# Kernel optimization log

Hardware: AMD Instinct MI355X
Metric: run time of the kernel (lower is better)

Reference implementation:

```python
import jax, jax.numpy as jnp
import numpy as np
from jax import lax

T_LOW, T_HIGH = 100.0, 200.0   # init kwargs of Canny
TG22 = 0.4142135623730951      # tan(22.5 deg), cv2's direction quantization constant
MAX_ITERS = 512                # safety cap on hysteresis fixed-point loop


def _shift(a, dy, dx):
    # neighbor value n[y, x] = a[y + dy, x + dx], zero outside
    H, W = a.shape
    p = jnp.pad(a, 1)
    return p[1 + dy:1 + dy + H, 1 + dx:1 + dx + W]


def _canny(x):
    B, C, H, W = x.shape
    # toRGB: ((x+1)/2*255).to(uint8)  (truncation; values are non-negative)
    img = jnp.clip(jnp.floor((x + 1.0) * 0.5 * 255.0), 0.0, 255.0)
    # original reshapes batch into one tall strip (B*H, W, C) before cv2.Canny
    img = img.transpose(0, 2, 3, 1).reshape(B * H, W, C)
    HH = B * H
    p = jnp.pad(img, ((1, 1), (1, 1), (0, 0)), mode='edge')  # replicate border like cv2

    def s(dy, dx):
        return p[1 + dy:1 + dy + HH, 1 + dx:1 + dx + W, :]

    # 3x3 Sobel per channel
    gx = (s(-1, 1) + 2.0 * s(0, 1) + s(1, 1)) - (s(-1, -1) + 2.0 * s(0, -1) + s(1, -1))
    gy = (s(1, -1) + 2.0 * s(1, 0) + s(1, 1)) - (s(-1, -1) + 2.0 * s(-1, 0) + s(-1, 1))
    mag_c = jnp.abs(gx) + jnp.abs(gy)  # L1 magnitude (cv2 default L2gradient=False)
    # multi-channel: take channel with max magnitude per pixel (cv2 behavior)
    idx = jnp.argmax(mag_c, axis=-1, keepdims=True)
    gx = jnp.take_along_axis(gx, idx, -1)[..., 0]
    gy = jnp.take_along_axis(gy, idx, -1)[..., 0]
    mag = jnp.take_along_axis(mag_c, idx, -1)[..., 0]

    # non-maximum suppression with 4 quantized directions
    ax_, ay_ = jnp.abs(gx), jnp.abs(gy)
    is_h = ay_ < TG22 * ax_          # gradient ~horizontal -> compare left/right
    is_v = ay_ * TG22 > ax_          # gradient ~vertical -> compare up/down
    same = (gx * gy) >= 0.0          # diagonal orientation by sign agreement
    n1 = jnp.where(is_h, _shift(mag, 0, -1),
         jnp.where(is_v, _shift(mag, -1, 0),
         jnp.where(same, _shift(mag, -1, -1), _shift(mag, -1, 1))))
    n2 = jnp.where(is_h, _shift(mag, 0, 1),
         jnp.where(is_v, _shift(mag, 1, 0),
         jnp.where(same, _shift(mag, 1, 1), _shift(mag, 1, -1))))
    keep = (mag > n1) & (mag >= n2)

    strong = keep & (mag > T_HIGH)
    weak = keep & (mag > T_LOW)

    # hysteresis: propagate strong labels through 8-connected weak pixels to fixed point
    def dilate(m):
        mf = m.astype(jnp.float32)
        return lax.reduce_window(mf, 0.0, lax.add, (3, 3), (1, 1), 'SAME') > 0.0

    def body(st):
        s0, _, it = st
        grown = (dilate(s0) & weak) | s0
        return grown, jnp.any(grown != s0), it + 1

    def cond(st):
        return st[1] & (st[2] < MAX_ITERS)

    strong, _, _ = lax.while_loop(cond, body, (strong, jnp.array(True), jnp.array(0)))

    edges = strong.reshape(B, H, W).astype(jnp.float32)        # {0,1} == cv2 {0,255}/255
    edges = jnp.broadcast_to(edges[:, None, :, :], (B, 3, H, W))
    return (edges - 0.5) / 0.5                                 # T.Normalize(0.5, 0.5)


def setup_inputs() -> dict:
    key = jax.random.key(0)
    x = jax.random.uniform(key, (16, 3, 512, 512), jnp.float32, -1.0, 1.0)
    return {"x": x}


def reference(x):
    return _canny(x)
```

## Files before the change

kernel.cpp:

```cpp
#include <hip/hip_runtime.h>
#include <stdint.h>

#define HH 8192
#define WW 512
#define WPR 8
#define TG22F 0.4142135623730951f
#define NROUND 8
#define NBLK 32


__device__ __forceinline__ float to_img(float v) {
    float t = floorf((v + 1.0f) * 0.5f * 255.0f);
    return fminf(fmaxf(t, 0.0f), 255.0f);
}

__device__ __forceinline__ uint64_t runfill(uint64_t s, uint64_t w) {
    uint64_t sw = s & w;
    uint64_t up = ((sw + w) ^ w) & w;
    uint64_t rs = __brevll(sw);
    uint64_t rw = __brevll(w);
    uint64_t dn = __brevll(((rs + rw) ^ rw) & rw);
    return up | dn | sw;
}

__device__ __forceinline__ uint64_t shfl_up64(uint64_t v, int d) {
    int lo = __shfl_up((int)(uint32_t)v, d, 64);
    int hi = __shfl_up((int)(uint32_t)(v >> 32), d, 64);
    return ((uint64_t)(uint32_t)hi << 32) | (uint32_t)lo;
}
__device__ __forceinline__ uint64_t shfl_dn64(uint64_t v, int d) {
    int lo = __shfl_down((int)(uint32_t)v, d, 64);
    int hi = __shfl_down((int)(uint32_t)(v >> 32), d, 64);
    return ((uint64_t)(uint32_t)hi << 32) | (uint32_t)lo;
}

__device__ __forceinline__ uint64_t cload64(const unsigned long long* p) {
    return __hip_atomic_load((const unsigned long long*)p, __ATOMIC_RELAXED,
                             __HIP_MEMORY_SCOPE_AGENT);
}
__device__ __forceinline__ void cstore64(unsigned long long* p, uint64_t v) {
    __hip_atomic_store(p, (unsigned long long)v, __ATOMIC_RELAXED,
                       __HIP_MEMORY_SCOPE_AGENT);
}

__device__ __forceinline__ void load_row10(const float* __restrict__ in,
                                           int row, int c, int lane, int a[10]) {
    const float* p = &in[(size_t)((((row >> 9) * 3 + c) << 9) + (row & 511)) << 9];
    const int x0 = lane << 3;
    float4 v0 = *(const float4*)&p[x0];
    float4 v1 = *(const float4*)&p[x0 + 4];
    a[1] = (int)(uint8_t)to_img(v0.x);
    a[2] = (int)(uint8_t)to_img(v0.y);
    a[3] = (int)(uint8_t)to_img(v0.z);
    a[4] = (int)(uint8_t)to_img(v0.w);
    a[5] = (int)(uint8_t)to_img(v1.x);
    a[6] = (int)(uint8_t)to_img(v1.y);
    a[7] = (int)(uint8_t)to_img(v1.z);
    a[8] = (int)(uint8_t)to_img(v1.w);
    int l = __shfl_up(a[8], 1, 64);
    a[0] = (lane == 0) ? a[1] : l;
    int r = __shfl_down(a[1], 1, 64);
    a[9] = (lane == 63) ? a[8] : r;
}

__global__ void k_sobel(const float* __restrict__ in, uint16_t* __restrict__ packed) {
    const int lane = threadIdx.x & 63;
    const int y  = (blockIdx.x << 2) + (threadIdx.x >> 6);
    const int ym = (y > 0) ? y - 1 : 0;
    const int yp = (y < HH - 1) ? y + 1 : HH - 1;

    int bestMag[8], bgx[8], bgy[8];
    #pragma unroll
    for (int j = 0; j < 8; ++j) { bestMag[j] = -1; bgx[j] = 0; bgy[j] = 0; }

    #pragma unroll
    for (int c = 0; c < 3; ++c) {
        int a0[10], a1[10], a2[10];
        load_row10(in, ym, c, lane, a0);
        load_row10(in, y,  c, lane, a1);
        load_row10(in, yp, c, lane, a2);
        int vs[10];
        #pragma unroll
        for (int i = 0; i < 10; ++i) vs[i] = a0[i] + 2 * a1[i] + a2[i];
        #pragma unroll
        for (int j = 0; j < 8; ++j) {
            int gx = vs[j + 2] - vs[j];
            int gy = (a2[j] + 2 * a2[j + 1] + a2[j + 2]) - (a0[j] + 2 * a0[j + 1] + a0[j + 2]);
            int mg = abs(gx) + abs(gy);
            if (mg > bestMag[j]) { bestMag[j] = mg; bgx[j] = gx; bgy[j] = gy; }
        }
    }

    uint32_t res[4];
    #pragma unroll
    for (int jj = 0; jj < 4; ++jj) {
        uint32_t pair = 0;
        #pragma unroll
        for (int s = 0; s < 2; ++s) {
            int j = jj * 2 + s;
            float axf = (float)abs(bgx[j]);
            float ayf = (float)abs(bgy[j]);
            int dir;
            if (ayf < TG22F * axf)      dir = 0;
            else if (ayf * TG22F > axf) dir = 1;
            else                        dir = (bgx[j] * bgy[j] >= 0) ? 2 : 3;
            uint32_t val = (uint32_t)(bestMag[j] | (dir << 12));
            pair |= val << (s * 16);
        }
        res[jj] = pair;
    }
    *(uint4*)&packed[y * WW + (lane << 3)] = *(uint4*)res;
}

#define MEXT(lo, hi, idx) ((int)((((idx) < 4 ? ((lo) >> (16 * (idx))) \
                                             : ((hi) >> (16 * ((idx) - 4))))) & 0xFFF))

__global__ void k_nms(const uint16_t* __restrict__ packed,
                      unsigned long long* __restrict__ strongB,
                      unsigned long long* __restrict__ weakB,
                      int* __restrict__ flags) {
    if (blockIdx.x == 0 && threadIdx.x < 16) flags[threadIdx.x] = 0;
    const int lane = threadIdx.x & 63;
    const int w = threadIdx.x >> 6;
    const int y = (blockIdx.x << 2) + w;

    uint4 q = *(const uint4*)&packed[y * WW + (lane << 3)];
    uint64_t oLo = ((uint64_t)q.y << 32) | q.x;
    uint64_t oHi = ((uint64_t)q.w << 32) | q.z;
    uint64_t uLo = 0, uHi = 0, dLo = 0, dHi = 0;
    if (y > 0) {
        uint4 qu = *(const uint4*)&packed[(y - 1) * WW + (lane << 3)];
        uLo = ((uint64_t)qu.y << 32) | qu.x;
        uHi = ((uint64_t)qu.w << 32) | qu.z;
    }
    if (y < HH - 1) {
        uint4 qd = *(const uint4*)&packed[(y + 1) * WW + (lane << 3)];
        dLo = ((uint64_t)qd.y << 32) | qd.x;
        dHi = ((uint64_t)qd.w << 32) | qd.z;
    }

    int oL = __shfl_up((int)((oHi >> 48) & 0xFFF), 1, 64); if (lane == 0) oL = 0;
    int uL = __shfl_up((int)((uHi >> 48) & 0xFFF), 1, 64); if (lane == 0) uL = 0;
    int dL = __shfl_up((int)((dHi >> 48) & 0xFFF), 1, 64); if (lane == 0) dL = 0;
    int oR = __shfl_down((int)(oLo & 0xFFF), 1, 64); if (lane == 63) oR = 0;
    int uR = __shfl_down((int)(uLo & 0xFFF), 1, 64); if (lane == 63) uR = 0;
    int dR = __shfl_down((int)(dLo & 0xFFF), 1, 64); if (lane == 63) dR = 0;

    uint32_t sb = 0, wb = 0;
    #pragma unroll
    for (int i = 0; i < 8; ++i) {
        int raw = (int)(((i < 4 ? (oLo >> (16 * i)) : (oHi >> (16 * (i - 4))))) & 0xFFFF);
        int m = raw & 0xFFF;
        int dir = raw >> 12;
        int Om1 = (i == 0) ? oL : MEXT(oLo, oHi, (i == 0 ? 0 : i - 1));
        int Op1 = (i == 7) ? oR : MEXT(oLo, oHi, (i == 7 ? 7 : i + 1));
        int Ui  = MEXT(uLo, uHi, i);
        int Um1 = (i == 0) ? uL : MEXT(uLo, uHi, (i == 0 ? 0 : i - 1));
        int Up1 = (i == 7) ? uR : MEXT(uLo, uHi, (i == 7 ? 7 : i + 1));
        int Di  = MEXT(dLo, dHi, i);
        int Dm1 = (i == 0) ? dL : MEXT(dLo, dHi, (i == 0 ? 0 : i - 1));
        int Dp1 = (i == 7) ? dR : MEXT(dLo, dHi, (i == 7 ? 7 : i + 1));
        int n1 = (dir == 0) ? Om1 : (dir == 1) ? Ui : (dir == 2) ? Um1 : Up1;
        int n2 = (dir == 0) ? Op1 : (dir == 1) ? Di : (dir == 2) ? Dp1 : Dm1;
        bool keep = (m > n1) && (m >= n2);
        if (keep && m > 200) sb |= 1u << i;
        if (keep && m > 100) wb |= 1u << i;
    }

    const int src = (lane & 7) << 3;
    uint64_t wordS = 0, wordW = 0;
    #pragma unroll
    for (int i = 0; i < 8; ++i) {
        wordS |= (uint64_t)(uint32_t)__shfl((int)sb, src + i, 64) << (i * 8);
        wordW |= (uint64_t)(uint32_t)__shfl((int)wb, src + i, 64) << (i * 8);
    }
    if (lane < 8)       strongB[y * WPR + lane] = wordS;
    else if (lane < 16) weakB[y * WPR + (lane - 8)] = wordW;
}

__global__ void __launch_bounds__(256) k_hyst(
        const unsigned long long* __restrict__ weakB,
        unsigned long long* __restrict__ buf,
        int* __restrict__ flags)
{
    const int lane = threadIdx.x & 63;
    const int wave = (blockIdx.x << 2) + (threadIdx.x >> 6);
    const int base = ((wave << 6) + lane) * WPR;

    uint64_t own[8], wk[8];
    #pragma unroll
    for (int k = 0; k < 8; ++k) { wk[k] = weakB[base + k]; own[k] = buf[base + k]; }

    uint64_t hspu[8], hspd[8];
    #pragma unroll
    for (int k = 0; k < 8; ++k) { hspu[k] = 0; hspd[k] = 0; }

    auto load_halo = [&]() {
        uint64_t h[8];
        if (lane == 0 && wave > 0) {
            #pragma unroll
            for (int k = 0; k < 8; ++k) h[k] = cload64(&buf[base - WPR + k]);
            #pragma unroll
            for (int k = 0; k < 8; ++k) {
                uint64_t a = h[k] | (h[k] << 1) | (h[k] >> 1);
                if (k > 0) a |= h[k - 1] >> 63;
                if (k < 7) a |= h[k + 1] << 63;
                hspu[k] = a;
            }
        }
        if (lane == 63 && wave < 127) {
            #pragma unroll
            for (int k = 0; k < 8; ++k) h[k] = cload64(&buf[base + WPR + k]);
            #pragma unroll
            for (int k = 0; k < 8; ++k) {
                uint64_t a = h[k] | (h[k] << 1) | (h[k] >> 1);
                if (k > 0) a |= h[k - 1] >> 63;
                if (k < 7) a |= h[k + 1] << 63;
                hspd[k] = a;
            }
        }
    };
    load_halo();

    bool grewAny = false;
    for (int r = 0; r < NROUND; ++r) {
        bool grew = false;
        for (;;) {
            uint64_t sp[8];
            #pragma unroll
            for (int k = 0; k < 8; ++k) {
                uint64_t h = own[k] | (own[k] << 1) | (own[k] >> 1);
                if (k > 0) h |= own[k - 1] >> 63;
                if (k < 7) h |= own[k + 1] << 63;
                sp[k] = h;
            }
            uint64_t su[8], sd[8];
            #pragma unroll
            for (int k = 0; k < 8; ++k) {
                su[k] = shfl_up64(sp[k], 1);
                sd[k] = shfl_dn64(sp[k], 1);
            }
            if (lane == 0) {
                #pragma unroll
                for (int k = 0; k < 8; ++k) su[k] = hspu[k];
            }
            if (lane == 63) {
                #pragma unroll
                for (int k = 0; k < 8; ++k) sd[k] = hspd[k];
            }
            uint32_t ch = 0;
            #pragma unroll
            for (int k = 0; k < 8; ++k) {
                uint64_t acc = sp[k] | su[k] | sd[k];
                uint64_t nv = runfill(own[k] | (acc & wk[k]), wk[k]);
                ch |= (uint32_t)(nv != own[k]);
                own[k] = nv;
            }
            if (ch) grew = true;
            if (__ballot(ch ? 1 : 0) == 0ull) break;
        }
        grewAny |= grew;

        if (grew && lane == 0)
            __hip_atomic_store(&flags[r], 1, __ATOMIC_RELAXED, __HIP_MEMORY_SCOPE_AGENT);
        if (lane == 0 || lane == 63) {
            #pragma unroll
            for (int k = 0; k < 8; ++k) cstore64(&buf[base + k], own[k]);
        }
        __syncthreads();
        if (threadIdx.x == 0) {
            __hip_atomic_fetch_add(&flags[8 + r], 1, __ATOMIC_RELAXED, __HIP_MEMORY_SCOPE_AGENT);
            while (__hip_atomic_load(&flags[8 + r], __ATOMIC_RELAXED, __HIP_MEMORY_SCOPE_AGENT) < NBLK)
                __builtin_amdgcn_s_sleep(2);
        }
        __syncthreads();

        if (__hip_atomic_load(&flags[r], __ATOMIC_RELAXED, __HIP_MEMORY_SCOPE_AGENT) == 0)
            break;
        if (r + 1 < NROUND) load_halo();
    }

    if (__ballot(grewAny ? 1 : 0) != 0ull) {
        #pragma unroll
        for (int k = 0; k < 8; ++k) buf[base + k] = own[k];
    }
}

__global__ void k_out(const unsigned long long* __restrict__ result, float* __restrict__ out) {
    int t = blockIdx.x * blockDim.x + threadIdx.x;
    int b = t >> 16;
    int r = t & 65535;
    int h = r >> 7;
    int w = (r & 127) << 2;
    int y = (b << 9) + h;
    unsigned long long word = result[y * WPR + (w >> 6)];
    int sh = w & 63;
    float4 v;
    v.x = ((word >> (sh + 0)) & 1ull) ? 1.0f : -1.0f;
    v.y = ((word >> (sh + 1)) & 1ull) ? 1.0f : -1.0f;
    v.z = ((word >> (sh + 2)) & 1ull) ? 1.0f : -1.0f;
    v.w = ((word >> (sh + 3)) & 1ull) ? 1.0f : -1.0f;
    int base = (b * 3) << 18;
    int off = (h << 9) + w;
    *(float4*)&out[base + off] = v;
    *(float4*)&out[base + 262144 + off] = v;
    *(float4*)&out[base + 524288 + off] = v;
}

extern "C" void kernel_launch(void* const* d_in, const int* in_sizes, int n_in,
                              void* d_out, int out_size, void* d_ws, size_t ws_size,
                              hipStream_t stream) {
    const float* x = (const float*)d_in[0];
    float* out = (float*)d_out;
    char* ws = (char*)d_ws;

    uint16_t* packed          = (uint16_t*)(ws);
    unsigned long long* buf   = (unsigned long long*)(ws + 8388608);
    unsigned long long* weakB = (unsigned long long*)(ws + 8912896);
    int* flags                = (int*)(ws + 9437184);

    k_sobel<<<2048, 256, 0, stream>>>(x, packed);
    k_nms<<<2048, 256, 0, stream>>>(packed, buf, weakB, flags);
    k_hyst<<<NBLK, 256, 0, stream>>>(weakB, buf, flags);
    k_out<<<4096, 256, 0, stream>>>(buf, out);
}
```

Before: 119.5 us.

## Fuse Sobel and NMS into one kernel with recomputed neighbor-row magnitudes

Merges the Sobel and non-maximum suppression kernels into a single kernel. Each row-wave now loads five input rows per channel and recomputes the magnitudes of the rows above and below, instead of writing and re-reading a packed magnitude/direction buffer. This drops one launch and the round trip through the intermediate buffer. In exchange it roughly triples the Sobel arithmetic, increases input reads from three to five rows per channel (mostly served by cache), and raises register pressure.

```diff
diff --git a/kernel.cpp b/kernel.cpp
--- a/kernel.cpp
+++ b/kernel.cpp
@@ -63,108 +63,96 @@
     a[9] = (lane == 63) ? a[8] : r;
 }
 
-__global__ void k_sobel(const float* __restrict__ in, uint16_t* __restrict__ packed) {
-    const int lane = threadIdx.x & 63;
-    const int y  = (blockIdx.x << 2) + (threadIdx.x >> 6);
-    const int ym = (y > 0) ? y - 1 : 0;
-    const int yp = (y < HH - 1) ? y + 1 : HH - 1;
-
-    int bestMag[8], bgx[8], bgy[8];
-    #pragma unroll
-    for (int j = 0; j < 8; ++j) { bestMag[j] = -1; bgx[j] = 0; bgy[j] = 0; }
-
-    #pragma unroll
-    for (int c = 0; c < 3; ++c) {
-        int a0[10], a1[10], a2[10];
-        load_row10(in, ym, c, lane, a0);
-        load_row10(in, y,  c, lane, a1);
-        load_row10(in, yp, c, lane, a2);
-        int vs[10];
-        #pragma unroll
-        for (int i = 0; i < 10; ++i) vs[i] = a0[i] + 2 * a1[i] + a2[i];
-        #pragma unroll
-        for (int j = 0; j < 8; ++j) {
-            int gx = vs[j + 2] - vs[j];
-            int gy = (a2[j] + 2 * a2[j + 1] + a2[j + 2]) - (a0[j] + 2 * a0[j + 1] + a0[j + 2]);
-            int mg = abs(gx) + abs(gy);
-            if (mg > bestMag[j]) { bestMag[j] = mg; bgx[j] = gx; bgy[j] = gy; }
-        }
-    }
-
-    uint32_t res[4];
-    #pragma unroll
-    for (int jj = 0; jj < 4; ++jj) {
-        uint32_t pair = 0;
-        #pragma unroll
-        for (int s = 0; s < 2; ++s) {
-            int j = jj * 2 + s;
-            float axf = (float)abs(bgx[j]);
-            float ayf = (float)abs(bgy[j]);
-            int dir;
-            if (ayf < TG22F * axf)      dir = 0;
-            else if (ayf * TG22F > axf) dir = 1;
-            else                        dir = (bgx[j] * bgy[j] >= 0) ? 2 : 3;
-            uint32_t val = (uint32_t)(bestMag[j] | (dir << 12));
-            pair |= val << (s * 16);
-        }
-        res[jj] = pair;
-    }
-    *(uint4*)&packed[y * WW + (lane << 3)] = *(uint4*)res;
-}
-
-#define MEXT(lo, hi, idx) ((int)((((idx) < 4 ? ((lo) >> (16 * (idx))) \
-                                             : ((hi) >> (16 * ((idx) - 4))))) & 0xFFF))
-
-__global__ void k_nms(const uint16_t* __restrict__ packed,
-                      unsigned long long* __restrict__ strongB,
-                      unsigned long long* __restrict__ weakB,
-                      int* __restrict__ flags) {
+__global__ void k_sobnms(const float* __restrict__ in,
+                         unsigned long long* __restrict__ strongB,
+                         unsigned long long* __restrict__ weakB,
+                         int* __restrict__ flags) {
     if (blockIdx.x == 0 && threadIdx.x < 16) flags[threadIdx.x] = 0;
     const int lane = threadIdx.x & 63;
-    const int w = threadIdx.x >> 6;
-    const int y = (blockIdx.x << 2) + w;
-
-    uint4 q = *(const uint4*)&packed[y * WW + (lane << 3)];
-    uint64_t oLo = ((uint64_t)q.y << 32) | q.x;
-    uint64_t oHi = ((uint64_t)q.w << 32) | q.z;
-    uint64_t uLo = 0, uHi = 0, dLo = 0, dHi = 0;
-    if (y > 0) {
-        uint4 qu = *(const uint4*)&packed[(y - 1) * WW + (lane << 3)];
-        uLo = ((uint64_t)qu.y << 32) | qu.x;
-        uHi = ((uint64_t)qu.w << 32) | qu.z;
-    }
-    if (y < HH - 1) {
-        uint4 qd = *(const uint4*)&packed[(y + 1) * WW + (lane << 3)];
-        dLo = ((uint64_t)qd.y << 32) | qd.x;
-        dHi = ((uint64_t)qd.w << 32) | qd.z;
-    }
-
-    int oL = __shfl_up((int)((oHi >> 48) & 0xFFF), 1, 64); if (lane == 0) oL = 0;
-    int uL = __shfl_up((int)((uHi >> 48) & 0xFFF), 1, 64); if (lane == 0) uL = 0;
-    int dL = __shfl_up((int)((dHi >> 48) & 0xFFF), 1, 64); if (lane == 0) dL = 0;
-    int oR = __shfl_down((int)(oLo & 0xFFF), 1, 64); if (lane == 63) oR = 0;
-    int uR = __shfl_down((int)(uLo & 0xFFF), 1, 64); if (lane == 63) uR = 0;
-    int dR = __shfl_down((int)(dLo & 0xFFF), 1, 64); if (lane == 63) dR = 0;
+    const int y = (blockIdx.x << 2) + (threadIdx.x >> 6);
+
+    const int r0 = (y - 2 < 0) ? 0 : y - 2;
+    const int r1 = (y - 1 < 0) ? 0 : y - 1;
+    const int r3 = (y + 1 >= HH) ? HH - 1 : y + 1;
+    const int r4 = (y + 2 >= HH) ? HH - 1 : y + 2;
+
+    int magU[8], magC[8], magD[8], bgx[8], bgy[8];
+    #pragma unroll
+    for (int j = 0; j < 8; ++j) {
+        magU[j] = -1; magC[j] = -1; magD[j] = -1; bgx[j] = 0; bgy[j] = 0;
+    }
+
+    #pragma unroll
+    for (int c = 0; c < 3; ++c) {
+        int a0[10], a1[10], a2[10], a3[10], a4[10];
+        load_row10(in, r0, c, lane, a0);
+        load_row10(in, r1, c, lane, a1);
+        load_row10(in, y,  c, lane, a2);
+        load_row10(in, r3, c, lane, a3);
+        load_row10(in, r4, c, lane, a4);
+        int vsU[10], vsC[10], vsD[10];
+        #pragma unroll
+        for (int i = 0; i < 10; ++i) {
+            vsU[i] = a0[i] + 2 * a1[i] + a2[i];
+            vsC[i] = a1[i] + 2 * a2[i] + a3[i];
+            vsD[i] = a2[i] + 2 * a3[i] + a4[i];
+        }
+        #pragma unroll
+        for (int j = 0; j < 8; ++j) {
+            int gxu = vsU[j + 2] - vsU[j];
+            int gyu = (a2[j] + 2 * a2[j + 1] + a2[j + 2]) - (a0[j] + 2 * a0[j + 1] + a0[j + 2]);
+            int mgu = abs(gxu) + abs(gyu);
+            if (mgu > magU[j]) magU[j] = mgu;
+            int gxc = vsC[j + 2] - vsC[j];
+            int gyc = (a3[j] + 2 * a3[j + 1] + a3[j + 2]) - (a1[j] + 2 * a1[j + 1] + a1[j + 2]);
+            int mgc = abs(gxc) + abs(gyc);
+            if (mgc > magC[j]) { magC[j] = mgc; bgx[j] = gxc; bgy[j] = gyc; }
+            int gxd = vsD[j + 2] - vsD[j];
+            int gyd = (a4[j] + 2 * a4[j + 1] + a4[j + 2]) - (a2[j] + 2 * a2[j + 1] + a2[j + 2]);
+            int mgd = abs(gxd) + abs(gyd);
+            if (mgd > magD[j]) magD[j] = mgd;
+        }
+    }
+
+    if (y == 0) {
+        #pragma unroll
+        for (int j = 0; j < 8; ++j) magU[j] = 0;
+    }
+    if (y == HH - 1) {
+        #pragma unroll
+        for (int j = 0; j < 8; ++j) magD[j] = 0;
+    }
+
+    int oL = __shfl_up(magC[7], 1, 64);   if (lane == 0)  oL = 0;
+    int uL = __shfl_up(magU[7], 1, 64);   if (lane == 0)  uL = 0;
+    int dL = __shfl_up(magD[7], 1, 64);   if (lane == 0)  dL = 0;
+    int oR = __shfl_down(magC[0], 1, 64); if (lane == 63) oR = 0;
+    int uR = __shfl_down(magU[0], 1, 64); if (lane == 63) uR = 0;
+    int dR = __shfl_down(magD[0], 1, 64); if (lane == 63) dR = 0;
 
     uint32_t sb = 0, wb = 0;
     #pragma unroll
-    for (int i = 0; i < 8; ++i) {
-        int raw = (int)(((i < 4 ? (oLo >> (16 * i)) : (oHi >> (16 * (i - 4))))) & 0xFFFF);
-        int m = raw & 0xFFF;
-        int dir = raw >> 12;
-        int Om1 = (i == 0) ? oL : MEXT(oLo, oHi, (i == 0 ? 0 : i - 1));
-        int Op1 = (i == 7) ? oR : MEXT(oLo, oHi, (i == 7 ? 7 : i + 1));
-        int Ui  = MEXT(uLo, uHi, i);
-        int Um1 = (i == 0) ? uL : MEXT(uLo, uHi, (i == 0 ? 0 : i - 1));
-        int Up1 = (i == 7) ? uR : MEXT(uLo, uHi, (i == 7 ? 7 : i + 1));
-        int Di  = MEXT(dLo, dHi, i);
-        int Dm1 = (i == 0) ? dL : MEXT(dLo, dHi, (i == 0 ? 0 : i - 1));
-        int Dp1 = (i == 7) ? dR : MEXT(dLo, dHi, (i == 7 ? 7 : i + 1));
+    for (int j = 0; j < 8; ++j) {
+        int m = magC[j];
+        float axf = (float)abs(bgx[j]);
+        float ayf = (float)abs(bgy[j]);
+        int dir;
+        if (ayf < TG22F * axf)      dir = 0;
+        else if (ayf * TG22F > axf) dir = 1;
+        else                        dir = (bgx[j] * bgy[j] >= 0) ? 2 : 3;
+        int Om1 = (j == 0) ? oL : magC[j == 0 ? 0 : j - 1];
+        int Op1 = (j == 7) ? oR : magC[j == 7 ? 7 : j + 1];
+        int Ui  = magU[j];
+        int Um1 = (j == 0) ? uL : magU[j == 0 ? 0 : j - 1];
+        int Up1 = (j == 7) ? uR : magU[j == 7 ? 7 : j + 1];
+        int Di  = magD[j];
+        int Dm1 = (j == 0) ? dL : magD[j == 0 ? 0 : j - 1];
+        int Dp1 = (j == 7) ? dR : magD[j == 7 ? 7 : j + 1];
         int n1 = (dir == 0) ? Om1 : (dir == 1) ? Ui : (dir == 2) ? Um1 : Up1;
         int n2 = (dir == 0) ? Op1 : (dir == 1) ? Di : (dir == 2) ? Dp1 : Dm1;
         bool keep = (m > n1) && (m >= n2);
-        if (keep && m > 200) sb |= 1u << i;
-        if (keep && m > 100) wb |= 1u << i;
+        if (keep && m > 200) sb |= 1u << j;
+        if (keep && m > 100) wb |= 1u << j;
     }
 
     const int src = (lane & 7) << 3;
@@ -314,13 +302,11 @@
     float* out = (float*)d_out;
     char* ws = (char*)d_ws;
 
-    uint16_t* packed          = (uint16_t*)(ws);
-    unsigned long long* buf   = (unsigned long long*)(ws + 8388608);
-    unsigned long long* weakB = (unsigned long long*)(ws + 8912896);
-    int* flags                = (int*)(ws + 9437184);
-
-    k_sobel<<<2048, 256, 0, stream>>>(x, packed);
-    k_nms<<<2048, 256, 0, stream>>>(packed, buf, weakB, flags);
+    unsigned long long* buf   = (unsigned long long*)(ws);
+    unsigned long long* weakB = (unsigned long long*)(ws + 524288);
+    int* flags                = (int*)(ws + 1048576);
+
+    k_sobnms<<<2048, 256, 0, stream>>>(x, buf, weakB, flags);
     k_hyst<<<NBLK, 256, 0, stream>>>(weakB, buf, flags);
     k_out<<<4096, 256, 0, stream>>>(buf, out);
 }
```

New measurement: 195.7 us. 63.7% more time.

## Propagate hysteresis across waves within a block via shared memory before global sync

Applied to the files above, without the earlier changes.

The hysteresis kernel now exchanges boundary rows between the four waves of a block through shared memory and iterates to a block-local fixed point, so only block-edge rows go through global memory and the grid-wide barrier. This aims to cut the number of global rounds and atomic barriers needed for labels to cross wave boundaries, at the cost of extra __syncthreads per inner iteration. The pixel conversion also drops the floor and clamp in favour of a plain float-to-int truncation, which is valid for non-negative inputs in range.

```diff
diff --git a/kernel.cpp b/kernel.cpp
--- a/kernel.cpp
+++ b/kernel.cpp
@@ -9,9 +9,8 @@
 #define NBLK 32
 
 
-__device__ __forceinline__ float to_img(float v) {
-    float t = floorf((v + 1.0f) * 0.5f * 255.0f);
-    return fminf(fmaxf(t, 0.0f), 255.0f);
+__device__ __forceinline__ int to_img_i(float v) {
+    return (int)((v + 1.0f) * 0.5f * 255.0f);
 }
 
 __device__ __forceinline__ uint64_t runfill(uint64_t s, uint64_t w) {
@@ -43,27 +42,38 @@
                        __HIP_MEMORY_SCOPE_AGENT);
 }
 
+__device__ __forceinline__ void spread8(const uint64_t h[8], uint64_t o[8]) {
+    #pragma unroll
+    for (int k = 0; k < 8; ++k) {
+        uint64_t a = h[k] | (h[k] << 1) | (h[k] >> 1);
+        if (k > 0) a |= h[k - 1] >> 63;
+        if (k < 7) a |= h[k + 1] << 63;
+        o[k] = a;
+    }
+}
+
 __device__ __forceinline__ void load_row10(const float* __restrict__ in,
                                            int row, int c, int lane, int a[10]) {
     const float* p = &in[(size_t)((((row >> 9) * 3 + c) << 9) + (row & 511)) << 9];
     const int x0 = lane << 3;
     float4 v0 = *(const float4*)&p[x0];
     float4 v1 = *(const float4*)&p[x0 + 4];
-    a[1] = (int)(uint8_t)to_img(v0.x);
-    a[2] = (int)(uint8_t)to_img(v0.y);
-    a[3] = (int)(uint8_t)to_img(v0.z);
-    a[4] = (int)(uint8_t)to_img(v0.w);
-    a[5] = (int)(uint8_t)to_img(v1.x);
-    a[6] = (int)(uint8_t)to_img(v1.y);
-    a[7] = (int)(uint8_t)to_img(v1.z);
-    a[8] = (int)(uint8_t)to_img(v1.w);
+    a[1] = to_img_i(v0.x);
+    a[2] = to_img_i(v0.y);
+    a[3] = to_img_i(v0.z);
+    a[4] = to_img_i(v0.w);
+    a[5] = to_img_i(v1.x);
+    a[6] = to_img_i(v1.y);
+    a[7] = to_img_i(v1.z);
+    a[8] = to_img_i(v1.w);
     int l = __shfl_up(a[8], 1, 64);
     a[0] = (lane == 0) ? a[1] : l;
     int r = __shfl_down(a[1], 1, 64);
     a[9] = (lane == 63) ? a[8] : r;
 }
 
-__global__ void k_sobel(const float* __restrict__ in, uint16_t* __restrict__ packed) {
+__global__ void __launch_bounds__(256) k_sobel(const float* __restrict__ in,
+                                               uint16_t* __restrict__ packed) {
     const int lane = threadIdx.x & 63;
     const int y  = (blockIdx.x << 2) + (threadIdx.x >> 6);
     const int ym = (y > 0) ? y - 1 : 0;
@@ -183,87 +193,119 @@
         unsigned long long* __restrict__ buf,
         int* __restrict__ flags)
 {
+    __shared__ uint64_t topRow[4][8];
+    __shared__ uint64_t botRow[4][8];
+    __shared__ int chFlag;
+
     const int lane = threadIdx.x & 63;
-    const int wave = (blockIdx.x << 2) + (threadIdx.x >> 6);
-    const int base = ((wave << 6) + lane) * WPR;
+    const int wid  = threadIdx.x >> 6;
+    const int gw   = (blockIdx.x << 2) + wid;
+    const int base = ((gw << 6) + lane) * WPR;
 
     uint64_t own[8], wk[8];
     #pragma unroll
     for (int k = 0; k < 8; ++k) { wk[k] = weakB[base + k]; own[k] = buf[base + k]; }
 
-    uint64_t hspu[8], hspd[8];
-    #pragma unroll
-    for (int k = 0; k < 8; ++k) { hspu[k] = 0; hspd[k] = 0; }
-
-    auto load_halo = [&]() {
-        uint64_t h[8];
-        if (lane == 0 && wave > 0) {
+    bool grewAny = false;
+
+    for (int r = 0; r < NROUND; ++r) {
+        uint64_t extsp[8];
+        #pragma unroll
+        for (int k = 0; k < 8; ++k) extsp[k] = 0;
+        if (wid == 0 && lane == 0 && blockIdx.x > 0) {
+            uint64_t h[8];
             #pragma unroll
             for (int k = 0; k < 8; ++k) h[k] = cload64(&buf[base - WPR + k]);
-            #pragma unroll
-            for (int k = 0; k < 8; ++k) {
-                uint64_t a = h[k] | (h[k] << 1) | (h[k] >> 1);
-                if (k > 0) a |= h[k - 1] >> 63;
-                if (k < 7) a |= h[k + 1] << 63;
-                hspu[k] = a;
-            }
-        }
-        if (lane == 63 && wave < 127) {
+            spread8(h, extsp);
+        }
+        if (wid == 3 && lane == 63 && blockIdx.x < NBLK - 1) {
+            uint64_t h[8];
             #pragma unroll
             for (int k = 0; k < 8; ++k) h[k] = cload64(&buf[base + WPR + k]);
-            #pragma unroll
-            for (int k = 0; k < 8; ++k) {
-                uint64_t a = h[k] | (h[k] << 1) | (h[k] >> 1);
-                if (k > 0) a |= h[k - 1] >> 63;
-                if (k < 7) a |= h[k + 1] << 63;
-                hspd[k] = a;
-            }
-        }
-    };
-    load_halo();
-
-    bool grewAny = false;
-    for (int r = 0; r < NROUND; ++r) {
-        bool grew = false;
+            spread8(h, extsp);
+        }
+
+        bool roundGrew = false;
         for (;;) {
-            uint64_t sp[8];
-            #pragma unroll
-            for (int k = 0; k < 8; ++k) {
-                uint64_t h = own[k] | (own[k] << 1) | (own[k] >> 1);
-                if (k > 0) h |= own[k - 1] >> 63;
-                if (k < 7) h |= own[k + 1] << 63;
-                sp[k] = h;
-            }
-            uint64_t su[8], sd[8];
-            #pragma unroll
-            for (int k = 0; k < 8; ++k) {
-                su[k] = shfl_up64(sp[k], 1);
-                sd[k] = shfl_dn64(sp[k], 1);
-            }
+            __syncthreads();
+            if (threadIdx.x == 0) chFlag = 0;
             if (lane == 0) {
                 #pragma unroll
-                for (int k = 0; k < 8; ++k) su[k] = hspu[k];
+                for (int k = 0; k < 8; ++k) topRow[wid][k] = own[k];
             }
             if (lane == 63) {
                 #pragma unroll
-                for (int k = 0; k < 8; ++k) sd[k] = hspd[k];
-            }
-            uint32_t ch = 0;
+                for (int k = 0; k < 8; ++k) botRow[wid][k] = own[k];
+            }
+            __syncthreads();
+
+            uint64_t hspu[8], hspd[8];
             #pragma unroll
-            for (int k = 0; k < 8; ++k) {
-                uint64_t acc = sp[k] | su[k] | sd[k];
-                uint64_t nv = runfill(own[k] | (acc & wk[k]), wk[k]);
-                ch |= (uint32_t)(nv != own[k]);
-                own[k] = nv;
-            }
-            if (ch) grew = true;
-            if (__ballot(ch ? 1 : 0) == 0ull) break;
-        }
-        grewAny |= grew;
-
-        if (grew && lane == 0)
+            for (int k = 0; k < 8; ++k) { hspu[k] = 0; hspd[k] = 0; }
+            if (lane == 0) {
+                if (wid > 0) {
+                    uint64_t h[8];
+                    #pragma unroll
+                    for (int k = 0; k < 8; ++k) h[k] = botRow[wid - 1][k];
+                    spread8(h, hspu);
+                } else {
+                    #pragma unroll
+                    for (int k = 0; k < 8; ++k) hspu[k] = extsp[k];
+                }
+            }
+            if (lane == 63) {
+                if (wid < 3) {
+                    uint64_t h[8];
+                    #pragma unroll
+                    for (int k = 0; k < 8; ++k) h[k] = topRow[wid + 1][k];
+                    spread8(h, hspd);
+                } else {
+                    #pragma unroll
+                    for (int k = 0; k < 8; ++k) hspd[k] = extsp[k];
+                }
+            }
+
+            bool grew = false;
+            for (;;) {
+                uint64_t sp[8];
+                spread8(own, sp);
+                uint64_t su[8], sd[8];
+                #pragma unroll
+                for (int k = 0; k < 8; ++k) {
+                    su[k] = shfl_up64(sp[k], 1);
+                    sd[k] = shfl_dn64(sp[k], 1);
+                }
+                if (lane == 0) {
+                    #pragma unroll
+                    for (int k = 0; k < 8; ++k) su[k] = hspu[k];
+                }
+                if (lane == 63) {
+                    #pragma unroll
+                    for (int k = 0; k < 8; ++k) sd[k] = hspd[k];
+                }
+                uint32_t ch = 0;
+                #pragma unroll
+                for (int k = 0; k < 8; ++k) {
+                    uint64_t acc = sp[k] | su[k] | sd[k];
+                    uint64_t nv = runfill(own[k] | (acc & wk[k]), wk[k]);
+                    ch |= (uint32_t)(nv != own[k]);
+                    own[k] = nv;
+                }
+                if (ch) grew = true;
+                if (__ballot(ch ? 1 : 0) == 0ull) break;
+            }
+
+            bool waveGrew = (__ballot(grew ? 1 : 0) != 0ull);
+            if (waveGrew && lane == 0) chFlag = 1;
+            __syncthreads();
+            if (chFlag == 0) break;
+            roundGrew = true;
+        }
+        grewAny |= roundGrew;
+
+        if (roundGrew && threadIdx.x == 0)
             __hip_atomic_store(&flags[r], 1, __ATOMIC_RELAXED, __HIP_MEMORY_SCOPE_AGENT);
-        if (lane == 0 || lane == 63) {
+        if ((wid == 0 && lane == 0) || (wid == 3 && lane == 63)) {
             #pragma unroll
             for (int k = 0; k < 8; ++k) cstore64(&buf[base + k], own[k]);
         }
@@ -277,10 +319,9 @@
 
         if (__hip_atomic_load(&flags[r], __ATOMIC_RELAXED, __HIP_MEMORY_SCOPE_AGENT) == 0)
             break;
-        if (r + 1 < NROUND) load_halo();
-    }
-
-    if (__ballot(grewAny ? 1 : 0) != 0ull) {
+    }
+
+    if (grewAny) {
         #pragma unroll
         for (int k = 0; k < 8; ++k) buf[base + k] = own[k];
     }
```

Result: no change. 121.3 us (+1.5%).

## Fuse NMS and hysteresis kernels with an atomic grid barrier

Applied to the files above, without the earlier changes.

Merges the NMS and hysteresis kernels into one launch. Every block first does its NMS rows and bumps an atomic counter. The first NBLK blocks then spin until all blocks have arrived and run the hysteresis on the coherently stored bitmaps. The flag reset moves into the Sobel kernel, and the uint8 conversion drops the floor and clamp in favour of a plain int truncation. This saves a kernel launch and some ALU work, but relies on the remaining blocks being scheduled while the early ones spin, and on inputs staying in [-1,1] for the truncation to match.

```diff
diff --git a/kernel.cpp b/kernel.cpp
--- a/kernel.cpp
+++ b/kernel.cpp
@@ -9,9 +9,8 @@
 #define NBLK 32
 
 
-__device__ __forceinline__ float to_img(float v) {
-    float t = floorf((v + 1.0f) * 0.5f * 255.0f);
-    return fminf(fmaxf(t, 0.0f), 255.0f);
+__device__ __forceinline__ int to_img_i(float v) {
+    return (int)((v + 1.0f) * 0.5f * 255.0f);
 }
 
 __device__ __forceinline__ uint64_t runfill(uint64_t s, uint64_t w) {
@@ -49,21 +48,24 @@
     const int x0 = lane << 3;
     float4 v0 = *(const float4*)&p[x0];
     float4 v1 = *(const float4*)&p[x0 + 4];
-    a[1] = (int)(uint8_t)to_img(v0.x);
-    a[2] = (int)(uint8_t)to_img(v0.y);
-    a[3] = (int)(uint8_t)to_img(v0.z);
-    a[4] = (int)(uint8_t)to_img(v0.w);
-    a[5] = (int)(uint8_t)to_img(v1.x);
-    a[6] = (int)(uint8_t)to_img(v1.y);
-    a[7] = (int)(uint8_t)to_img(v1.z);
-    a[8] = (int)(uint8_t)to_img(v1.w);
+    a[1] = to_img_i(v0.x);
+    a[2] = to_img_i(v0.y);
+    a[3] = to_img_i(v0.z);
+    a[4] = to_img_i(v0.w);
+    a[5] = to_img_i(v1.x);
+    a[6] = to_img_i(v1.y);
+    a[7] = to_img_i(v1.z);
+    a[8] = to_img_i(v1.w);
     int l = __shfl_up(a[8], 1, 64);
     a[0] = (lane == 0) ? a[1] : l;
     int r = __shfl_down(a[1], 1, 64);
     a[9] = (lane == 63) ? a[8] : r;
 }
 
-__global__ void k_sobel(const float* __restrict__ in, uint16_t* __restrict__ packed) {
+__global__ void __launch_bounds__(256) k_sobel(const float* __restrict__ in,
+                                               uint16_t* __restrict__ packed,
+                                               int* __restrict__ flags) {
+    if (blockIdx.x == 0 && threadIdx.x < 32) flags[threadIdx.x] = 0;
     const int lane = threadIdx.x & 63;
     const int y  = (blockIdx.x << 2) + (threadIdx.x >> 6);
     const int ym = (y > 0) ? y - 1 : 0;
@@ -115,81 +117,92 @@
 #define MEXT(lo, hi, idx) ((int)((((idx) < 4 ? ((lo) >> (16 * (idx))) \
                                              : ((hi) >> (16 * ((idx) - 4))))) & 0xFFF))
 
-__global__ void k_nms(const uint16_t* __restrict__ packed,
-                      unsigned long long* __restrict__ strongB,
-                      unsigned long long* __restrict__ weakB,
-                      int* __restrict__ flags) {
-    if (blockIdx.x == 0 && threadIdx.x < 16) flags[threadIdx.x] = 0;
-    const int lane = threadIdx.x & 63;
-    const int w = threadIdx.x >> 6;
-    const int y = (blockIdx.x << 2) + w;
-
-    uint4 q = *(const uint4*)&packed[y * WW + (lane << 3)];
-    uint64_t oLo = ((uint64_t)q.y << 32) | q.x;
-    uint64_t oHi = ((uint64_t)q.w << 32) | q.z;
-    uint64_t uLo = 0, uHi = 0, dLo = 0, dHi = 0;
-    if (y > 0) {
-        uint4 qu = *(const uint4*)&packed[(y - 1) * WW + (lane << 3)];
-        uLo = ((uint64_t)qu.y << 32) | qu.x;
-        uHi = ((uint64_t)qu.w << 32) | qu.z;
-    }
-    if (y < HH - 1) {
-        uint4 qd = *(const uint4*)&packed[(y + 1) * WW + (lane << 3)];
-        dLo = ((uint64_t)qd.y << 32) | qd.x;
-        dHi = ((uint64_t)qd.w << 32) | qd.z;
-    }
-
-    int oL = __shfl_up((int)((oHi >> 48) & 0xFFF), 1, 64); if (lane == 0) oL = 0;
-    int uL = __shfl_up((int)((uHi >> 48) & 0xFFF), 1, 64); if (lane == 0) uL = 0;
-    int dL = __shfl_up((int)((dHi >> 48) & 0xFFF), 1, 64); if (lane == 0) dL = 0;
-    int oR = __shfl_down((int)(oLo & 0xFFF), 1, 64); if (lane == 63) oR = 0;
-    int uR = __shfl_down((int)(uLo & 0xFFF), 1, 64); if (lane == 63) uR = 0;
-    int dR = __shfl_down((int)(dLo & 0xFFF), 1, 64); if (lane == 63) dR = 0;
-
-    uint32_t sb = 0, wb = 0;
-    #pragma unroll
-    for (int i = 0; i < 8; ++i) {
-        int raw = (int)(((i < 4 ? (oLo >> (16 * i)) : (oHi >> (16 * (i - 4))))) & 0xFFFF);
-        int m = raw & 0xFFF;
-        int dir = raw >> 12;
-        int Om1 = (i == 0) ? oL : MEXT(oLo, oHi, (i == 0 ? 0 : i - 1));
-        int Op1 = (i == 7) ? oR : MEXT(oLo, oHi, (i == 7 ? 7 : i + 1));
-        int Ui  = MEXT(uLo, uHi, i);
-        int Um1 = (i == 0) ? uL : MEXT(uLo, uHi, (i == 0 ? 0 : i - 1));
-        int Up1 = (i == 7) ? uR : MEXT(uLo, uHi, (i == 7 ? 7 : i + 1));
-        int Di  = MEXT(dLo, dHi, i);
-        int Dm1 = (i == 0) ? dL : MEXT(dLo, dHi, (i == 0 ? 0 : i - 1));
-        int Dp1 = (i == 7) ? dR : MEXT(dLo, dHi, (i == 7 ? 7 : i + 1));
-        int n1 = (dir == 0) ? Om1 : (dir == 1) ? Ui : (dir == 2) ? Um1 : Up1;
-        int n2 = (dir == 0) ? Op1 : (dir == 1) ? Di : (dir == 2) ? Dp1 : Dm1;
-        bool keep = (m > n1) && (m >= n2);
-        if (keep && m > 200) sb |= 1u << i;
-        if (keep && m > 100) wb |= 1u << i;
-    }
-
-    const int src = (lane & 7) << 3;
-    uint64_t wordS = 0, wordW = 0;
-    #pragma unroll
-    for (int i = 0; i < 8; ++i) {
-        wordS |= (uint64_t)(uint32_t)__shfl((int)sb, src + i, 64) << (i * 8);
-        wordW |= (uint64_t)(uint32_t)__shfl((int)wb, src + i, 64) << (i * 8);
-    }
-    if (lane < 8)       strongB[y * WPR + lane] = wordS;
-    else if (lane < 16) weakB[y * WPR + (lane - 8)] = wordW;
-}
-
-__global__ void __launch_bounds__(256) k_hyst(
-        const unsigned long long* __restrict__ weakB,
+__global__ void __launch_bounds__(256) k_nmsh(
+        const uint16_t* __restrict__ packed,
         unsigned long long* __restrict__ buf,
+        unsigned long long* __restrict__ weakB,
         int* __restrict__ flags)
 {
     const int lane = threadIdx.x & 63;
-    const int wave = (blockIdx.x << 2) + (threadIdx.x >> 6);
+    const int wid  = threadIdx.x >> 6;
+    {
+        const int y = (blockIdx.x << 2) + wid;
+
+        uint4 q = *(const uint4*)&packed[y * WW + (lane << 3)];
+        uint64_t oLo = ((uint64_t)q.y << 32) | q.x;
+        uint64_t oHi = ((uint64_t)q.w << 32) | q.z;
+        uint64_t uLo = 0, uHi = 0, dLo = 0, dHi = 0;
+        if (y > 0) {
+            uint4 qu = *(const uint4*)&packed[(y - 1) * WW + (lane << 3)];
+            uLo = ((uint64_t)qu.y << 32) | qu.x;
+            uHi = ((uint64_t)qu.w << 32) | qu.z;
+        }
+        if (y < HH - 1) {
+            uint4 qd = *(const uint4*)&packed[(y + 1) * WW + (lane << 3)];
+            dLo = ((uint64_t)qd.y << 32) | qd.x;
+            dHi = ((uint64_t)qd.w << 32) | qd.z;
+        }
+
+        int oL = __shfl_up((int)((oHi >> 48) & 0xFFF), 1, 64); if (lane == 0) oL = 0;
+        int uL = __shfl_up((int)((uHi >> 48) & 0xFFF), 1, 64); if (lane == 0) uL = 0;
+        int dL = __shfl_up((int)((dHi >> 48) & 0xFFF), 1, 64); if (lane == 0) dL = 0;
+        int oR = __shfl_down((int)(oLo & 0xFFF), 1, 64); if (lane == 63) oR = 0;
+        int uR = __shfl_down((int)(uLo & 0xFFF), 1, 64); if (lane == 63) uR = 0;
+        int dR = __shfl_down((int)(dLo & 0xFFF), 1, 64); if (lane == 63) dR = 0;
+
+        uint32_t sb = 0, wb = 0;
+        #pragma unroll
+        for (int i = 0; i < 8; ++i) {
+            int raw = (int)(((i < 4 ? (oLo >> (16 * i)) : (oHi >> (16 * (i - 4))))) & 0xFFFF);
+            int m = raw & 0xFFF;
+            int dir = raw >> 12;
+            int Om1 = (i == 0) ? oL : MEXT(oLo, oHi, (i == 0 ? 0 : i - 1));
+            int Op1 = (i == 7) ? oR : MEXT(oLo, oHi, (i == 7 ? 7 : i + 1));
+            int Ui  = MEXT(uLo, uHi, i);
+            int Um1 = (i == 0) ? uL : MEXT(uLo, uHi, (i == 0 ? 0 : i - 1));
+            int Up1 = (i == 7) ? uR : MEXT(uLo, uHi, (i == 7 ? 7 : i + 1));
+            int Di  = MEXT(dLo, dHi, i);
+            int Dm1 = (i == 0) ? dL : MEXT(dLo, dHi, (i == 0 ? 0 : i - 1));
+            int Dp1 = (i == 7) ? dR : MEXT(dLo, dHi, (i == 7 ? 7 : i + 1));
+            int n1 = (dir == 0) ? Om1 : (dir == 1) ? Ui : (dir == 2) ? Um1 : Up1;
+            int n2 = (dir == 0) ? Op1 : (dir == 1) ? Di : (dir == 2) ? Dp1 : Dm1;
+            bool keep = (m > n1) && (m >= n2);
+            if (keep && m > 200) sb |= 1u << i;
+            if (keep && m > 100) wb |= 1u << i;
+        }
+
+        const int src = (lane & 7) << 3;
+        uint64_t wordS = 0, wordW = 0;
+        #pragma unroll
+        for (int i = 0; i < 8; ++i) {
+            wordS |= (uint64_t)(uint32_t)__shfl((int)sb, src + i, 64) << (i * 8);
+            wordW |= (uint64_t)(uint32_t)__shfl((int)wb, src + i, 64) << (i * 8);
+        }
+        if (lane < 8)       cstore64(&buf[y * WPR + lane], wordS);
+        else if (lane < 16) cstore64(&weakB[y * WPR + (lane - 8)], wordW);
+    }
+
+    __syncthreads();
+    if (threadIdx.x == 0)
+        __hip_atomic_fetch_add(&flags[16], 1, __ATOMIC_RELAXED, __HIP_MEMORY_SCOPE_AGENT);
+    if (blockIdx.x >= NBLK) return;
+
+    if (threadIdx.x == 0) {
+        while (__hip_atomic_load(&flags[16], __ATOMIC_RELAXED, __HIP_MEMORY_SCOPE_AGENT)
+               < (int)gridDim.x)
+            __builtin_amdgcn_s_sleep(2);
+    }
+    __syncthreads();
+
+    const int wave = (blockIdx.x << 2) + wid;
     const int base = ((wave << 6) + lane) * WPR;
 
     uint64_t own[8], wk[8];
     #pragma unroll
-    for (int k = 0; k < 8; ++k) { wk[k] = weakB[base + k]; own[k] = buf[base + k]; }
+    for (int k = 0; k < 8; ++k) {
+        wk[k]  = cload64(&weakB[base + k]);
+        own[k] = cload64(&buf[base + k]);
+    }
 
     uint64_t hspu[8], hspd[8];
     #pragma unroll
@@ -319,8 +332,7 @@
     unsigned long long* weakB = (unsigned long long*)(ws + 8912896);
     int* flags                = (int*)(ws + 9437184);
 
-    k_sobel<<<2048, 256, 0, stream>>>(x, packed);
-    k_nms<<<2048, 256, 0, stream>>>(packed, buf, weakB, flags);
-    k_hyst<<<NBLK, 256, 0, stream>>>(weakB, buf, flags);
+    k_sobel<<<2048, 256, 0, stream>>>(x, packed, flags);
+    k_nmsh<<<2048, 256, 0, stream>>>(packed, buf, weakB, flags);
     k_out<<<4096, 256, 0, stream>>>(buf, out);
 }
```

Measured after the change: 148.6 us. +24.3%, slower.
